# Kernel optimization log

Hardware: AMD Instinct MI355X
Metric: run time of the kernel (lower is better)

## Reference

```python
import jax, jax.numpy as jnp
import numpy as np

N = 262144      # total nodes (2048 graphs x 128 nodes)
NA = 131072     # ally nodes (64 per graph)
D = 64          # feat_dim
K = 10          # num_clusters
B = 2048        # num graphs in batch
H = 64          # q_b_net hidden
VERY_SMALL_NUMBER = 1e-10


def setup_inputs() -> dict:
    key = jax.random.key(0)
    ks = jax.random.split(key, 8)
    node_feature = jax.random.normal(ks[0], (N, D), dtype=jnp.float32)
    qs = jax.random.normal(ks[1], (NA,), dtype=jnp.float32)
    # allies are the even-indexed nodes -> exactly 64 allies per 128-node graph
    ally_indices = jnp.arange(NA, dtype=jnp.int32) * 2
    node_graph_ids = jnp.arange(N, dtype=jnp.int32) // (N // B)
    # w_net head: node_feature -> per-cluster scores
    Ww = jax.random.normal(ks[2], (D, K), dtype=jnp.float32) * 0.1
    bw = jnp.zeros((K,), dtype=jnp.float32)
    # q_b_net MLP: sum_node_feature -> baseline q per cluster
    W1 = jax.random.normal(ks[3], (D, H), dtype=jnp.float32) * 0.1
    b1 = jnp.zeros((H,), dtype=jnp.float32)
    W2 = jax.random.normal(ks[4], (H, K), dtype=jnp.float32) * 0.1
    b2 = jnp.zeros((K,), dtype=jnp.float32)
    return {"node_feature": node_feature, "qs": qs, "Ww": Ww, "bw": bw,
            "W1": W1, "b1": b1, "W2": W2, "b2": b2,
            "ally_indices": ally_indices, "node_graph_ids": node_graph_ids}


def reference(node_feature, qs, Ww, bw, W1, b1, W2, b2, ally_indices, node_graph_ids):
    ally_seg = node_graph_ids[ally_indices]                      # [NA] graph id of each ally

    # --- get_w: w_net scores, gather allies, clip, softmax over clusters ---
    ws_all = node_feature @ Ww + bw                              # [N, K]
    ally_ws = jnp.clip(ws_all[ally_indices], VERY_SMALL_NUMBER, 10.0)
    ally_ws = jax.nn.softmax(ally_ws, axis=1)                    # [NA, K]

    # --- get_feat ---
    ally_nf = node_feature[ally_indices]                         # [NA, D]
    # weighted_feat = ws[n,1,K] * nf[n,D,1]; per-graph sum replaces zero-scatter + dgl.sum_nodes
    weighted_feat = ally_ws[:, None, :] * ally_nf[:, :, None]    # [NA, D, K]
    wf_bdk = jax.ops.segment_sum(weighted_feat, ally_seg, num_segments=B)  # [B, D, K]
    wf = jnp.swapaxes(wf_bdk, 1, 2)                              # [B, K, D]
    # repeat_interleave(wf, num_ally_nodes) == gather by ally graph id
    repeat_wf = wf[ally_seg]                                     # [NA, K, D]
    group_dot = jnp.einsum('nd,nkd->nk', ally_nf, repeat_wf)     # [NA, K]
    nf_norm = jnp.linalg.norm(ally_nf, axis=1, keepdims=True)    # [NA, 1]
    wf_norm = jnp.linalg.norm(repeat_wf, axis=2)                 # [NA, K]
    ally_normed = group_dot / (nf_norm * wf_norm)                # [NA, K]
    normed_full = jnp.zeros((node_feature.shape[0], K), node_feature.dtype)
    normed_full = normed_full.at[ally_indices].set(ally_normed)  # [N, K]

    # --- get_q ---
    weighted_q = qs[:, None] * ally_ws                           # [NA, K]
    q_agg = jax.ops.segment_sum(weighted_q, ally_seg, num_segments=B)      # [B, K]
    sum_nf = jax.ops.segment_sum(node_feature, node_graph_ids, num_segments=B)  # [B, D]
    q_v = jax.nn.relu(sum_nf @ W1 + b1) @ W2 + b2                # [B, K]
    q_agg = q_agg + q_v

    return (q_agg, ally_ws, wf, ally_normed, normed_full)
```

## Files before the change

kernel.cpp:

```cpp
#include <hip/hip_runtime.h>


#define GK 10

#define OFF_QAGG   0
#define OFF_WS     20480
#define OFF_WF     1331200
#define OFF_NORMED 2641920
#define OFF_FULL   3952640

typedef __attribute__((ext_vector_type(4))) float f32x4;
typedef __attribute__((ext_vector_type(8))) short short8;

__device__ __forceinline__ unsigned short f2bf(float f) {
    unsigned u = __builtin_bit_cast(unsigned, f);
    u += 0x7FFFu + ((u >> 16) & 1u);
    return (unsigned short)(u >> 16);
}
__device__ __forceinline__ float bf2f(unsigned short h) {
    unsigned u = ((unsigned)h) << 16;
    return __builtin_bit_cast(float, u);
}

__global__ __launch_bounds__(256, 4) void qmixer_kernel(
    const float* __restrict__ nf, const float* __restrict__ qs,
    const float* __restrict__ Ww, const float* __restrict__ bw,
    const float* __restrict__ W1, const float* __restrict__ b1,
    const float* __restrict__ W2, const float* __restrict__ b2,
    float* __restrict__ out)
{
    const int t    = threadIdx.x;
    const int lane = t & 63;
    const int wave = t >> 6;
    const int g    = wave >> 1;
    const int wl   = wave & 1;
    const int G    = 2 * blockIdx.x + g;

    __shared__ unsigned short s_Arm[2][64 * 72];
    __shared__ unsigned short s_wT[2][16 * 72];
    __shared__ unsigned short s_wscm[2][16 * 72];
    __shared__ float  s_sc[2][640];
    __shared__ float4 s_red4[2][2][16];
    __shared__ float  s_sumnf[2][64];
    __shared__ float  s_infn[2][64];
    __shared__ float  s_iwfn[2][16];
    __shared__ float  s_qagg[2][16];
    __shared__ float  s_qv[2][16];
    __shared__ float  s_hid[2][64];
    __shared__ float  s_qs[2][64];
    __shared__ float  s_bw[16];

    {
        const float4* nf4 = (const float4*)(nf + (size_t)G * 8192);
        const int tl   = t & 127;
        const int col4 = tl & 15;
        const int rgrp = tl >> 4;
        float4 cs = make_float4(0.f, 0.f, 0.f, 0.f);
#pragma unroll
        for (int i = 0; i < 16; ++i) {
            int row = rgrp * 16 + i;
            float4 v = nf4[row * 16 + col4];
            cs.x += v.x; cs.y += v.y; cs.z += v.z; cs.w += v.w;
            if ((i & 1) == 0) {
                const int a = row >> 1;
                ushort4 h;
                h.x = f2bf(v.x); h.y = f2bf(v.y); h.z = f2bf(v.z); h.w = f2bf(v.w);
                *(ushort4*)&s_Arm[g][a * 72 + col4 * 4] = h;
            }
        }
        cs.x += __shfl_xor(cs.x, 16); cs.y += __shfl_xor(cs.y, 16);
        cs.z += __shfl_xor(cs.z, 16); cs.w += __shfl_xor(cs.w, 16);
        cs.x += __shfl_xor(cs.x, 32); cs.y += __shfl_xor(cs.y, 32);
        cs.z += __shfl_xor(cs.z, 32); cs.w += __shfl_xor(cs.w, 32);
        if (lane < 16) s_red4[g][wl][lane] = cs;

        if (t < 160) {
            float4 wv = ((const float4*)Ww)[t];
            const float wa[4] = {wv.x, wv.y, wv.z, wv.w};
#pragma unroll
            for (int j = 0; j < 4; ++j) {
                int idx = t * 4 + j;
                int d = idx / 10, k = idx - d * 10;
                unsigned short hv = f2bf(wa[j]);
                s_wT[0][k * 72 + d] = hv;
                s_wT[1][k * 72 + d] = hv;
            }
        }
        for (int i = t; i < 432; i += 256) {
            s_wT[0][720 + i] = 0; s_wT[1][720 + i] = 0;
            s_wscm[0][720 + i] = 0; s_wscm[1][720 + i] = 0;
        }
        if (t < 128) s_qs[t >> 6][t & 63] = qs[(2 * blockIdx.x + (t >> 6)) * 64 + (t & 63)];
        if (t < 16)  s_bw[t] = (t < GK) ? bw[t] : 0.f;
    }
    __syncthreads();

    {
        const int mrow = lane & 15;
        const int kq   = lane >> 4;
        const int boff = mrow * 72 + kq * 8;
        short8 b0 = *(const short8*)&s_wT[g][boff];
        short8 b1 = *(const short8*)&s_wT[g][boff + 32];
#pragma unroll
        for (int i = 0; i < 2; ++i) {
            const int trow = wl * 32 + i * 16;
            const int aoff = (trow + mrow) * 72 + kq * 8;
            short8 a0 = *(const short8*)&s_Arm[g][aoff];
            short8 a1 = *(const short8*)&s_Arm[g][aoff + 32];
            f32x4 acc = {0.f, 0.f, 0.f, 0.f};
            acc = __builtin_amdgcn_mfma_f32_16x16x32_bf16(a0, b0, acc, 0, 0, 0);
            acc = __builtin_amdgcn_mfma_f32_16x16x32_bf16(a1, b1, acc, 0, 0, 0);
            if (mrow < GK) {
#pragma unroll
                for (int r = 0; r < 4; ++r)
                    s_sc[g][(trow + kq * 4 + r) * GK + mrow] = acc[r];
            }
            f32x4 nn = {0.f, 0.f, 0.f, 0.f};
            nn = __builtin_amdgcn_mfma_f32_16x16x32_bf16(a0, a0, nn, 0, 0, 0);
            nn = __builtin_amdgcn_mfma_f32_16x16x32_bf16(a1, a1, nn, 0, 0, 0);
            if (kq == (mrow >> 2)) {
                const int r3 = mrow & 3;
                float dv = (r3 == 0) ? nn[0] : (r3 == 1) ? nn[1] : (r3 == 2) ? nn[2] : nn[3];
                s_infn[g][trow + mrow] = rsqrtf(dv);
            }
        }
    }
    __syncthreads();

    if (wl == 0) {
        const int a = lane;
        float v[GK];
        float m = -1e30f;
#pragma unroll
        for (int k = 0; k < GK; ++k) {
            float x = fminf(fmaxf(s_sc[g][a * GK + k] + s_bw[k], 1e-10f), 10.f);
            v[k] = x; m = fmaxf(m, x);
        }
        float s = 0.f;
#pragma unroll
        for (int k = 0; k < GK; ++k) { v[k] = __expf(v[k] - m); s += v[k]; }
        float inv = 1.0f / s;
#pragma unroll
        for (int k = 0; k < GK; ++k)
            s_wscm[g][k * 72 + a] = f2bf(v[k] * inv);
    } else {
        const int j = lane;
        const float* rg = (const float*)&s_red4[g][0][0];
        float sn = rg[j] + rg[64 + j];
        s_sumnf[g][j] = sn;
        float acc = b1[j];
#pragma unroll
        for (int d4 = 0; d4 < 16; ++d4) {
            float4 s4 = *(const float4*)&s_sumnf[g][d4 * 4];
            acc += s4.x * W1[(d4 * 4 + 0) * 64 + j];
            acc += s4.y * W1[(d4 * 4 + 1) * 64 + j];
            acc += s4.z * W1[(d4 * 4 + 2) * 64 + j];
            acc += s4.w * W1[(d4 * 4 + 3) * 64 + j];
        }
        s_hid[g][j] = fmaxf(acc, 0.f);
    }
    __syncthreads();

    {
        const int nl15 = lane & 15;
        const int kq   = lane >> 4;
        const int aoff = nl15 * 72 + kq * 8;
        short8 a0 = *(const short8*)&s_wscm[g][aoff];
        short8 a1 = *(const short8*)&s_wscm[g][aoff + 32];
        float* o_wf = out + OFF_WF + (size_t)G * 640;
#pragma unroll
        for (int i = 0; i < 2; ++i) {
            const int dcol = wl * 32 + i * 16 + nl15;
            short8 b0, b1;
#pragma unroll
            for (int j = 0; j < 8; ++j) {
                b0[j] = (short)s_Arm[g][(kq * 8 + j) * 72 + dcol];
                b1[j] = (short)s_Arm[g][(kq * 8 + j + 32) * 72 + dcol];
            }
            f32x4 acc = {0.f, 0.f, 0.f, 0.f};
            acc = __builtin_amdgcn_mfma_f32_16x16x32_bf16(a0, b0, acc, 0, 0, 0);
            acc = __builtin_amdgcn_mfma_f32_16x16x32_bf16(a1, b1, acc, 0, 0, 0);
#pragma unroll
            for (int r = 0; r < 4; ++r) {
                const int kcl = kq * 4 + r;
                if (kcl < GK) {
                    o_wf[kcl * 64 + dcol]    = acc[r];
                    s_wT[g][kcl * 72 + dcol] = f2bf(acc[r]);
                }
            }
        }
    }
    __syncthreads();

    {
        const int mrow = lane & 15;
        const int kq   = lane >> 4;
        const int boff = mrow * 72 + kq * 8;
        short8 b0 = *(const short8*)&s_wT[g][boff];
        short8 b1 = *(const short8*)&s_wT[g][boff + 32];
        {
            f32x4 nn = {0.f, 0.f, 0.f, 0.f};
            nn = __builtin_amdgcn_mfma_f32_16x16x32_bf16(b0, b0, nn, 0, 0, 0);
            nn = __builtin_amdgcn_mfma_f32_16x16x32_bf16(b1, b1, nn, 0, 0, 0);
            if ((kq == (mrow >> 2)) && mrow < GK) {
                const int r3 = mrow & 3;
                float dv = (r3 == 0) ? nn[0] : (r3 == 1) ? nn[1] : (r3 == 2) ? nn[2] : nn[3];
                s_iwfn[g][mrow] = rsqrtf(dv);
            }
        }
        float iw = (mrow < GK) ? s_iwfn[g][mrow] : 0.f;
#pragma unroll
        for (int i = 0; i < 2; ++i) {
            const int trow = wl * 32 + i * 16;
            const int aoff = (trow + mrow) * 72 + kq * 8;
            short8 a0 = *(const short8*)&s_Arm[g][aoff];
            short8 a1 = *(const short8*)&s_Arm[g][aoff + 32];
            f32x4 acc = {0.f, 0.f, 0.f, 0.f};
            acc = __builtin_amdgcn_mfma_f32_16x16x32_bf16(a0, b0, acc, 0, 0, 0);
            acc = __builtin_amdgcn_mfma_f32_16x16x32_bf16(a1, b1, acc, 0, 0, 0);
            if (mrow < GK) {
                float4 if4 = *(const float4*)&s_infn[g][trow + kq * 4];
                const float ifa[4] = {if4.x, if4.y, if4.z, if4.w};
#pragma unroll
                for (int r = 0; r < 4; ++r)
                    s_sc[g][(trow + kq * 4 + r) * GK + mrow] = acc[r] * ifa[r] * iw;
            }
        }
        if (wl == 1) {
            if (lane < 40) {
                const int k  = lane >> 2;
                const int ap = lane & 3;
                float acc2 = 0.f;
#pragma unroll
                for (int a = ap * 16; a < ap * 16 + 16; ++a)
                    acc2 += s_qs[g][a] * bf2f(s_wscm[g][k * 72 + a]);
                acc2 += __shfl_xor(acc2, 1);
                acc2 += __shfl_xor(acc2, 2);
                if (ap == 0) s_qagg[g][k] = acc2;
            } else if (lane < 60) {
                const int k  = (lane - 40) >> 1;
                const int ap = (lane - 40) & 1;
                float acc2 = 0.f;
#pragma unroll
                for (int j = ap * 32; j < ap * 32 + 32; ++j)
                    acc2 += s_hid[g][j] * W2[j * GK + k];
                acc2 += __shfl_xor(acc2, 1);
                if (ap == 0) s_qv[g][k] = acc2;
            }
        }
    }
    __syncthreads();

    {
        const int tl = t & 127;
        float* o_norm = out + OFF_NORMED + (size_t)G * 640;
        float* o_ws   = out + OFF_WS + (size_t)G * 640;
        for (int e = tl; e < 640; e += 128) {
            int a = e / 10, k = e - a * 10;
            o_norm[e] = s_sc[g][e];
            o_ws[e]   = bf2f(s_wscm[g][k * 72 + a]);
        }
        float* o_full = out + OFF_FULL + (size_t)G * 1280;
        for (int e = tl; e < 1280; e += 128) {
            int row = e / 10, k = e - row * 10;
            float v = ((row & 1) == 0) ? s_sc[g][(row >> 1) * 10 + k] : 0.f;
            o_full[e] = v;
        }
        if (tl < GK)
            out[OFF_QAGG + (size_t)G * GK + tl] = s_qagg[g][tl] + s_qv[g][tl] + b2[tl];
    }
}

extern "C" void kernel_launch(void* const* d_in, const int* in_sizes, int n_in,
                              void* d_out, int out_size, void* d_ws, size_t ws_size,
                              hipStream_t stream) {
    const float* nf = (const float*)d_in[0];
    const float* qs = (const float*)d_in[1];
    const float* Ww = (const float*)d_in[2];
    const float* bw = (const float*)d_in[3];
    const float* W1 = (const float*)d_in[4];
    const float* b1 = (const float*)d_in[5];
    const float* W2 = (const float*)d_in[6];
    const float* b2 = (const float*)d_in[7];
    float* out = (float*)d_out;
    qmixer_kernel<<<dim3(1024), dim3(256), 0, stream>>>(nf, qs, Ww, bw, W1, b1, W2, b2, out);
}
```

Before: 122.3 us.

## Process two graphs sequentially per block with prefetch of second graph's features

Each 256-thread block now works through its two graphs one after the other, instead of splitting into two 128-thread halves that each handle one graph. The second graph's node features are prefetched into registers during the first graph's compute phases. The transposed-B operand gather is replaced by an explicit LDS transpose done by the otherwise idle waves. Barriers are custom s_barrier calls with an explicit lgkmcnt wait. This hides global load latency behind compute and gives each MFMA phase one tile per wave, but it doubles the number of serialized barrier phases and raises register pressure from the prefetched values.

Measured after the change: 216.8 us. +77.3%, slower.

```diff
diff --git a/kernel.cpp b/kernel.cpp
--- a/kernel.cpp
+++ b/kernel.cpp
@@ -20,6 +20,13 @@
 __device__ __forceinline__ float bf2f(unsigned short h) {
     unsigned u = ((unsigned)h) << 16;
     return __builtin_bit_cast(float, u);
+}
+
+__device__ __forceinline__ void phase_barrier() {
+    __builtin_amdgcn_sched_barrier(0);
+    asm volatile("s_waitcnt lgkmcnt(0)" ::: "memory");
+    __builtin_amdgcn_s_barrier();
+    __builtin_amdgcn_sched_barrier(0);
 }
 
 __global__ __launch_bounds__(256, 4) void qmixer_kernel(
@@ -32,47 +39,48 @@
     const int t    = threadIdx.x;
     const int lane = t & 63;
     const int wave = t >> 6;
-    const int g    = wave >> 1;
-    const int wl   = wave & 1;
-    const int G    = 2 * blockIdx.x + g;
-
-    __shared__ unsigned short s_Arm[2][64 * 72];
-    __shared__ unsigned short s_wT[2][16 * 72];
-    __shared__ unsigned short s_wscm[2][16 * 72];
-    __shared__ float  s_sc[2][640];
-    __shared__ float4 s_red4[2][2][16];
-    __shared__ float  s_sumnf[2][64];
-    __shared__ float  s_infn[2][64];
-    __shared__ float  s_iwfn[2][16];
-    __shared__ float  s_qagg[2][16];
-    __shared__ float  s_qv[2][16];
-    __shared__ float  s_hid[2][64];
+    const int bid  = blockIdx.x;
+    const int col4 = t & 15;
+    const int rgrp = t >> 4;
+
+    __shared__ unsigned short s_Arm [64 * 72];
+    __shared__ unsigned short s_ArmT[64 * 72];
+    __shared__ unsigned short s_wwT [16 * 72];
+    __shared__ unsigned short s_wfT [16 * 72];
+    __shared__ unsigned short s_wscm[16 * 72];
+    __shared__ float  s_sc[640];
+    __shared__ float4 s_red4[4][16];
+    __shared__ float  s_sumnf[64];
+    __shared__ float  s_infn[64];
+    __shared__ float  s_iwfn[16];
+    __shared__ float  s_qagg[16];
+    __shared__ float  s_qv[16];
+    __shared__ float  s_hid[64];
     __shared__ float  s_qs[2][64];
     __shared__ float  s_bw[16];
 
+    const float4* nf4a = (const float4*)(nf + (size_t)(2 * bid) * 8192);
+    const float4* nf4b = (const float4*)(nf + (size_t)(2 * bid + 1) * 8192);
+
     {
-        const float4* nf4 = (const float4*)(nf + (size_t)G * 8192);
-        const int tl   = t & 127;
-        const int col4 = tl & 15;
-        const int rgrp = tl >> 4;
         float4 cs = make_float4(0.f, 0.f, 0.f, 0.f);
 #pragma unroll
-        for (int i = 0; i < 16; ++i) {
-            int row = rgrp * 16 + i;
-            float4 v = nf4[row * 16 + col4];
+        for (int i = 0; i < 8; ++i) {
+            const int row = rgrp * 8 + i;
+            float4 v = nf4a[row * 16 + col4];
             cs.x += v.x; cs.y += v.y; cs.z += v.z; cs.w += v.w;
             if ((i & 1) == 0) {
                 const int a = row >> 1;
                 ushort4 h;
                 h.x = f2bf(v.x); h.y = f2bf(v.y); h.z = f2bf(v.z); h.w = f2bf(v.w);
-                *(ushort4*)&s_Arm[g][a * 72 + col4 * 4] = h;
+                *(ushort4*)&s_Arm[a * 72 + col4 * 4] = h;
             }
         }
         cs.x += __shfl_xor(cs.x, 16); cs.y += __shfl_xor(cs.y, 16);
         cs.z += __shfl_xor(cs.z, 16); cs.w += __shfl_xor(cs.w, 16);
         cs.x += __shfl_xor(cs.x, 32); cs.y += __shfl_xor(cs.y, 32);
         cs.z += __shfl_xor(cs.z, 32); cs.w += __shfl_xor(cs.w, 32);
-        if (lane < 16) s_red4[g][wl][lane] = cs;
+        if (lane < 16) s_red4[wave][lane] = cs;
 
         if (t < 160) {
             float4 wv = ((const float4*)Ww)[t];
@@ -81,39 +89,46 @@
             for (int j = 0; j < 4; ++j) {
                 int idx = t * 4 + j;
                 int d = idx / 10, k = idx - d * 10;
-                unsigned short hv = f2bf(wa[j]);
-                s_wT[0][k * 72 + d] = hv;
-                s_wT[1][k * 72 + d] = hv;
+                s_wwT[k * 72 + d] = f2bf(wa[j]);
             }
         }
         for (int i = t; i < 432; i += 256) {
-            s_wT[0][720 + i] = 0; s_wT[1][720 + i] = 0;
-            s_wscm[0][720 + i] = 0; s_wscm[1][720 + i] = 0;
-        }
-        if (t < 128) s_qs[t >> 6][t & 63] = qs[(2 * blockIdx.x + (t >> 6)) * 64 + (t & 63)];
+            s_wwT[720 + i] = 0; s_wfT[720 + i] = 0; s_wscm[720 + i] = 0;
+        }
+        if (t < 128) s_qs[t >> 6][t & 63] = qs[(size_t)(2 * bid + (t >> 6)) * 64 + (t & 63)];
         if (t < 16)  s_bw[t] = (t < GK) ? bw[t] : 0.f;
     }
-    __syncthreads();
-
-    {
-        const int mrow = lane & 15;
-        const int kq   = lane >> 4;
-        const int boff = mrow * 72 + kq * 8;
-        short8 b0 = *(const short8*)&s_wT[g][boff];
-        short8 b1 = *(const short8*)&s_wT[g][boff + 32];
-#pragma unroll
-        for (int i = 0; i < 2; ++i) {
-            const int trow = wl * 32 + i * 16;
+    phase_barrier();
+
+    float4 pf0, pf1, pf2, pf3;
+
+    for (int gg = 0; gg < 2; ++gg) {
+        const int G = 2 * bid + gg;
+
+        if (gg == 0) {
+            pf0 = nf4b[(rgrp * 8 + 0) * 16 + col4];
+            pf1 = nf4b[(rgrp * 8 + 2) * 16 + col4];
+            pf2 = nf4b[(rgrp * 8 + 4) * 16 + col4];
+            pf3 = nf4b[(rgrp * 8 + 6) * 16 + col4];
+        }
+
+        {
+            const int mrow = lane & 15;
+            const int kq   = lane >> 4;
+            const int trow = wave * 16;
+            const int boff = mrow * 72 + kq * 8;
+            short8 b0 = *(const short8*)&s_wwT[boff];
+            short8 b1 = *(const short8*)&s_wwT[boff + 32];
             const int aoff = (trow + mrow) * 72 + kq * 8;
-            short8 a0 = *(const short8*)&s_Arm[g][aoff];
-            short8 a1 = *(const short8*)&s_Arm[g][aoff + 32];
+            short8 a0 = *(const short8*)&s_Arm[aoff];
+            short8 a1 = *(const short8*)&s_Arm[aoff + 32];
             f32x4 acc = {0.f, 0.f, 0.f, 0.f};
             acc = __builtin_amdgcn_mfma_f32_16x16x32_bf16(a0, b0, acc, 0, 0, 0);
             acc = __builtin_amdgcn_mfma_f32_16x16x32_bf16(a1, b1, acc, 0, 0, 0);
             if (mrow < GK) {
 #pragma unroll
                 for (int r = 0; r < 4; ++r)
-                    s_sc[g][(trow + kq * 4 + r) * GK + mrow] = acc[r];
+                    s_sc[(trow + kq * 4 + r) * GK + mrow] = acc[r];
             }
             f32x4 nn = {0.f, 0.f, 0.f, 0.f};
             nn = __builtin_amdgcn_mfma_f32_16x16x32_bf16(a0, a0, nn, 0, 0, 0);
@@ -121,153 +136,185 @@
             if (kq == (mrow >> 2)) {
                 const int r3 = mrow & 3;
                 float dv = (r3 == 0) ? nn[0] : (r3 == 1) ? nn[1] : (r3 == 2) ? nn[2] : nn[3];
-                s_infn[g][trow + mrow] = rsqrtf(dv);
-            }
-        }
-    }
-    __syncthreads();
-
-    if (wl == 0) {
-        const int a = lane;
-        float v[GK];
-        float m = -1e30f;
-#pragma unroll
-        for (int k = 0; k < GK; ++k) {
-            float x = fminf(fmaxf(s_sc[g][a * GK + k] + s_bw[k], 1e-10f), 10.f);
-            v[k] = x; m = fmaxf(m, x);
-        }
-        float s = 0.f;
-#pragma unroll
-        for (int k = 0; k < GK; ++k) { v[k] = __expf(v[k] - m); s += v[k]; }
-        float inv = 1.0f / s;
-#pragma unroll
-        for (int k = 0; k < GK; ++k)
-            s_wscm[g][k * 72 + a] = f2bf(v[k] * inv);
-    } else {
-        const int j = lane;
-        const float* rg = (const float*)&s_red4[g][0][0];
-        float sn = rg[j] + rg[64 + j];
-        s_sumnf[g][j] = sn;
-        float acc = b1[j];
-#pragma unroll
-        for (int d4 = 0; d4 < 16; ++d4) {
-            float4 s4 = *(const float4*)&s_sumnf[g][d4 * 4];
-            acc += s4.x * W1[(d4 * 4 + 0) * 64 + j];
-            acc += s4.y * W1[(d4 * 4 + 1) * 64 + j];
-            acc += s4.z * W1[(d4 * 4 + 2) * 64 + j];
-            acc += s4.w * W1[(d4 * 4 + 3) * 64 + j];
-        }
-        s_hid[g][j] = fmaxf(acc, 0.f);
-    }
-    __syncthreads();
-
-    {
-        const int nl15 = lane & 15;
-        const int kq   = lane >> 4;
-        const int aoff = nl15 * 72 + kq * 8;
-        short8 a0 = *(const short8*)&s_wscm[g][aoff];
-        short8 a1 = *(const short8*)&s_wscm[g][aoff + 32];
-        float* o_wf = out + OFF_WF + (size_t)G * 640;
-#pragma unroll
-        for (int i = 0; i < 2; ++i) {
-            const int dcol = wl * 32 + i * 16 + nl15;
-            short8 b0, b1;
-#pragma unroll
-            for (int j = 0; j < 8; ++j) {
-                b0[j] = (short)s_Arm[g][(kq * 8 + j) * 72 + dcol];
-                b1[j] = (short)s_Arm[g][(kq * 8 + j + 32) * 72 + dcol];
-            }
+                s_infn[trow + mrow] = rsqrtf(dv);
+            }
+        }
+        phase_barrier();
+
+        if (wave == 0) {
+            const int a = lane;
+            float v[GK];
+            float m = -1e30f;
+#pragma unroll
+            for (int k = 0; k < GK; ++k) {
+                float x = fminf(fmaxf(s_sc[a * GK + k] + s_bw[k], 1e-10f), 10.f);
+                v[k] = x; m = fmaxf(m, x);
+            }
+            float s = 0.f;
+#pragma unroll
+            for (int k = 0; k < GK; ++k) { v[k] = __expf(v[k] - m); s += v[k]; }
+            float inv = 1.0f / s;
+#pragma unroll
+            for (int k = 0; k < GK; ++k)
+                s_wscm[k * 72 + a] = f2bf(v[k] * inv);
+        } else if (wave == 1) {
+            const int j = lane;
+            const float* rg = (const float*)&s_red4[0][0];
+            float sn = rg[j] + rg[64 + j] + rg[128 + j] + rg[192 + j];
+            s_sumnf[j] = sn;
+            float acc = b1[j];
+#pragma unroll
+            for (int d4 = 0; d4 < 16; ++d4) {
+                float4 s4 = *(const float4*)&s_sumnf[d4 * 4];
+                acc += s4.x * W1[(d4 * 4 + 0) * 64 + j];
+                acc += s4.y * W1[(d4 * 4 + 1) * 64 + j];
+                acc += s4.z * W1[(d4 * 4 + 2) * 64 + j];
+                acc += s4.w * W1[(d4 * 4 + 3) * 64 + j];
+            }
+            s_hid[j] = fmaxf(acc, 0.f);
+        } else {
+            const int a    = lane;
+            const int dblk = wave & 1;
+#pragma unroll
+            for (int w = 0; w < 4; ++w) {
+                short8 s = *(const short8*)&s_Arm[a * 72 + dblk * 32 + w * 8];
+#pragma unroll
+                for (int j = 0; j < 8; ++j)
+                    s_ArmT[(dblk * 32 + w * 8 + j) * 72 + a] = (unsigned short)s[j];
+            }
+        }
+        phase_barrier();
+
+        {
+            const int nl15 = lane & 15;
+            const int kq   = lane >> 4;
+            const int dcol = wave * 16 + nl15;
+            short8 a0 = *(const short8*)&s_wscm[nl15 * 72 + kq * 8];
+            short8 a1 = *(const short8*)&s_wscm[nl15 * 72 + kq * 8 + 32];
+            short8 b0 = *(const short8*)&s_ArmT[dcol * 72 + kq * 8];
+            short8 b1 = *(const short8*)&s_ArmT[dcol * 72 + kq * 8 + 32];
             f32x4 acc = {0.f, 0.f, 0.f, 0.f};
             acc = __builtin_amdgcn_mfma_f32_16x16x32_bf16(a0, b0, acc, 0, 0, 0);
             acc = __builtin_amdgcn_mfma_f32_16x16x32_bf16(a1, b1, acc, 0, 0, 0);
+            float* o_wf = out + OFF_WF + (size_t)G * 640;
 #pragma unroll
             for (int r = 0; r < 4; ++r) {
                 const int kcl = kq * 4 + r;
                 if (kcl < GK) {
-                    o_wf[kcl * 64 + dcol]    = acc[r];
-                    s_wT[g][kcl * 72 + dcol] = f2bf(acc[r]);
+                    o_wf[kcl * 64 + dcol]  = acc[r];
+                    s_wfT[kcl * 72 + dcol] = f2bf(acc[r]);
                 }
             }
         }
-    }
-    __syncthreads();
-
-    {
-        const int mrow = lane & 15;
-        const int kq   = lane >> 4;
-        const int boff = mrow * 72 + kq * 8;
-        short8 b0 = *(const short8*)&s_wT[g][boff];
-        short8 b1 = *(const short8*)&s_wT[g][boff + 32];
+        phase_barrier();
+
+        float4 od0, od1, od2, od3;
         {
-            f32x4 nn = {0.f, 0.f, 0.f, 0.f};
-            nn = __builtin_amdgcn_mfma_f32_16x16x32_bf16(b0, b0, nn, 0, 0, 0);
-            nn = __builtin_amdgcn_mfma_f32_16x16x32_bf16(b1, b1, nn, 0, 0, 0);
-            if ((kq == (mrow >> 2)) && mrow < GK) {
-                const int r3 = mrow & 3;
-                float dv = (r3 == 0) ? nn[0] : (r3 == 1) ? nn[1] : (r3 == 2) ? nn[2] : nn[3];
-                s_iwfn[g][mrow] = rsqrtf(dv);
-            }
-        }
-        float iw = (mrow < GK) ? s_iwfn[g][mrow] : 0.f;
-#pragma unroll
-        for (int i = 0; i < 2; ++i) {
-            const int trow = wl * 32 + i * 16;
+            if (gg == 0) {
+                od0 = nf4b[(rgrp * 8 + 1) * 16 + col4];
+                od1 = nf4b[(rgrp * 8 + 3) * 16 + col4];
+                od2 = nf4b[(rgrp * 8 + 5) * 16 + col4];
+                od3 = nf4b[(rgrp * 8 + 7) * 16 + col4];
+            }
+            const int mrow = lane & 15;
+            const int kq   = lane >> 4;
+            const int trow = wave * 16;
+            const int boff = mrow * 72 + kq * 8;
+            short8 b0 = *(const short8*)&s_wfT[boff];
+            short8 b1 = *(const short8*)&s_wfT[boff + 32];
+            {
+                f32x4 nn = {0.f, 0.f, 0.f, 0.f};
+                nn = __builtin_amdgcn_mfma_f32_16x16x32_bf16(b0, b0, nn, 0, 0, 0);
+                nn = __builtin_amdgcn_mfma_f32_16x16x32_bf16(b1, b1, nn, 0, 0, 0);
+                if ((kq == (mrow >> 2)) && mrow < GK) {
+                    const int r3 = mrow & 3;
+                    float dv = (r3 == 0) ? nn[0] : (r3 == 1) ? nn[1] : (r3 == 2) ? nn[2] : nn[3];
+                    s_iwfn[mrow] = rsqrtf(dv);
+                }
+            }
+            float iw = (mrow < GK) ? s_iwfn[mrow] : 0.f;
             const int aoff = (trow + mrow) * 72 + kq * 8;
-            short8 a0 = *(const short8*)&s_Arm[g][aoff];
-            short8 a1 = *(const short8*)&s_Arm[g][aoff + 32];
+            short8 a0 = *(const short8*)&s_Arm[aoff];
+            short8 a1 = *(const short8*)&s_Arm[aoff + 32];
             f32x4 acc = {0.f, 0.f, 0.f, 0.f};
             acc = __builtin_amdgcn_mfma_f32_16x16x32_bf16(a0, b0, acc, 0, 0, 0);
             acc = __builtin_amdgcn_mfma_f32_16x16x32_bf16(a1, b1, acc, 0, 0, 0);
             if (mrow < GK) {
-                float4 if4 = *(const float4*)&s_infn[g][trow + kq * 4];
+                float4 if4 = *(const float4*)&s_infn[trow + kq * 4];
                 const float ifa[4] = {if4.x, if4.y, if4.z, if4.w};
 #pragma unroll
                 for (int r = 0; r < 4; ++r)
-                    s_sc[g][(trow + kq * 4 + r) * GK + mrow] = acc[r] * ifa[r] * iw;
-            }
-        }
-        if (wl == 1) {
-            if (lane < 40) {
-                const int k  = lane >> 2;
-                const int ap = lane & 3;
-                float acc2 = 0.f;
-#pragma unroll
-                for (int a = ap * 16; a < ap * 16 + 16; ++a)
-                    acc2 += s_qs[g][a] * bf2f(s_wscm[g][k * 72 + a]);
-                acc2 += __shfl_xor(acc2, 1);
-                acc2 += __shfl_xor(acc2, 2);
-                if (ap == 0) s_qagg[g][k] = acc2;
-            } else if (lane < 60) {
-                const int k  = (lane - 40) >> 1;
-                const int ap = (lane - 40) & 1;
-                float acc2 = 0.f;
-#pragma unroll
-                for (int j = ap * 32; j < ap * 32 + 32; ++j)
-                    acc2 += s_hid[g][j] * W2[j * GK + k];
-                acc2 += __shfl_xor(acc2, 1);
-                if (ap == 0) s_qv[g][k] = acc2;
-            }
-        }
-    }
-    __syncthreads();
-
-    {
-        const int tl = t & 127;
-        float* o_norm = out + OFF_NORMED + (size_t)G * 640;
-        float* o_ws   = out + OFF_WS + (size_t)G * 640;
-        for (int e = tl; e < 640; e += 128) {
-            int a = e / 10, k = e - a * 10;
-            o_norm[e] = s_sc[g][e];
-            o_ws[e]   = bf2f(s_wscm[g][k * 72 + a]);
-        }
-        float* o_full = out + OFF_FULL + (size_t)G * 1280;
-        for (int e = tl; e < 1280; e += 128) {
-            int row = e / 10, k = e - row * 10;
-            float v = ((row & 1) == 0) ? s_sc[g][(row >> 1) * 10 + k] : 0.f;
-            o_full[e] = v;
-        }
-        if (tl < GK)
-            out[OFF_QAGG + (size_t)G * GK + tl] = s_qagg[g][tl] + s_qv[g][tl] + b2[tl];
+                    s_sc[(trow + kq * 4 + r) * GK + mrow] = acc[r] * ifa[r] * iw;
+            }
+            if (wave == 3) {
+                if (lane < 40) {
+                    const int k  = lane >> 2;
+                    const int ap = lane & 3;
+                    float acc2 = 0.f;
+#pragma unroll
+                    for (int a = ap * 16; a < ap * 16 + 16; ++a)
+                        acc2 += s_qs[gg][a] * bf2f(s_wscm[k * 72 + a]);
+                    acc2 += __shfl_xor(acc2, 1);
+                    acc2 += __shfl_xor(acc2, 2);
+                    if (ap == 0) s_qagg[k] = acc2;
+                } else if (lane < 60) {
+                    const int k  = (lane - 40) >> 1;
+                    const int ap = (lane - 40) & 1;
+                    float acc2 = 0.f;
+#pragma unroll
+                    for (int j = ap * 32; j < ap * 32 + 32; ++j)
+                        acc2 += s_hid[j] * W2[j * GK + k];
+                    acc2 += __shfl_xor(acc2, 1);
+                    if (ap == 0) s_qv[k] = acc2;
+                }
+            }
+        }
+        phase_barrier();
+
+        {
+            float* o_norm = out + OFF_NORMED + (size_t)G * 640;
+            float* o_ws   = out + OFF_WS + (size_t)G * 640;
+#pragma unroll
+            for (int e = t; e < 640; e += 256) {
+                int a = e / 10, k = e - a * 10;
+                o_norm[e] = s_sc[e];
+                o_ws[e]   = bf2f(s_wscm[k * 72 + a]);
+            }
+            float* o_full = out + OFF_FULL + (size_t)G * 1280;
+#pragma unroll
+            for (int e = t; e < 1280; e += 256) {
+                int row = e / 10, k = e - row * 10;
+                float v = ((row & 1) == 0) ? s_sc[(row >> 1) * 10 + k] : 0.f;
+                o_full[e] = v;
+            }
+            if (t < GK)
+                out[OFF_QAGG + (size_t)G * GK + t] = s_qagg[t] + s_qv[t] + b2[t];
+
+            if (gg == 0) {
+                float4 cs;
+                cs.x = pf0.x + pf1.x + pf2.x + pf3.x + od0.x + od1.x + od2.x + od3.x;
+                cs.y = pf0.y + pf1.y + pf2.y + pf3.y + od0.y + od1.y + od2.y + od3.y;
+                cs.z = pf0.z + pf1.z + pf2.z + pf3.z + od0.z + od1.z + od2.z + od3.z;
+                cs.w = pf0.w + pf1.w + pf2.w + pf3.w + od0.w + od1.w + od2.w + od3.w;
+
+                ushort4 h;
+                h.x = f2bf(pf0.x); h.y = f2bf(pf0.y); h.z = f2bf(pf0.z); h.w = f2bf(pf0.w);
+                *(ushort4*)&s_Arm[(rgrp * 4 + 0) * 72 + col4 * 4] = h;
+                h.x = f2bf(pf1.x); h.y = f2bf(pf1.y); h.z = f2bf(pf1.z); h.w = f2bf(pf1.w);
+                *(ushort4*)&s_Arm[(rgrp * 4 + 1) * 72 + col4 * 4] = h;
+                h.x = f2bf(pf2.x); h.y = f2bf(pf2.y); h.z = f2bf(pf2.z); h.w = f2bf(pf2.w);
+                *(ushort4*)&s_Arm[(rgrp * 4 + 2) * 72 + col4 * 4] = h;
+                h.x = f2bf(pf3.x); h.y = f2bf(pf3.y); h.z = f2bf(pf3.z); h.w = f2bf(pf3.w);
+                *(ushort4*)&s_Arm[(rgrp * 4 + 3) * 72 + col4 * 4] = h;
+
+                cs.x += __shfl_xor(cs.x, 16); cs.y += __shfl_xor(cs.y, 16);
+                cs.z += __shfl_xor(cs.z, 16); cs.w += __shfl_xor(cs.w, 16);
+                cs.x += __shfl_xor(cs.x, 32); cs.y += __shfl_xor(cs.y, 32);
+                cs.z += __shfl_xor(cs.z, 32); cs.w += __shfl_xor(cs.w, 32);
+                if (lane < 16) s_red4[wave][lane] = cs;
+            }
+        }
+        phase_barrier();
     }
 }
 
```
